# Kernel tuning notes

Hardware: AMD Instinct MI355X
Metric: run time of the kernel (lower is better)

## Reference

```python
import itertools
import jax, jax.numpy as jnp
import numpy as np

N_FEATURES = 32
DEGREE = 3
BATCH = 32768


def poly_feature_indices(n_features: int, degree: int):
    indices = []
    for d in range(1, degree + 1):
        for combo in itertools.combinations_with_replacement(range(n_features), d):
            indices.append(combo)
    return indices


def padded_index_matrix(n_features: int, degree: int) -> np.ndarray:
    # Pad each monomial index tuple to length `degree` with the sentinel
    # index n_features, which points at a column of ones appended to x.
    idx_list = poly_feature_indices(n_features, degree)
    mat = np.full((len(idx_list), degree), n_features, dtype=np.int32)
    for i, tup in enumerate(idx_list):
        mat[i, : len(tup)] = tup
    return mat


def setup_inputs() -> dict:
    key = jax.random.key(0)
    k1, k2, k3 = jax.random.split(key, 3)
    n_poly = len(poly_feature_indices(N_FEATURES, DEGREE))  # 6544
    x = jax.random.normal(k1, (BATCH, N_FEATURES), dtype=jnp.float32)
    # nn.Linear(n_poly, 1) init scale
    bound = 1.0 / np.sqrt(n_poly)
    W = jax.random.uniform(k2, (1, n_poly), dtype=jnp.float32, minval=-bound, maxval=bound)
    b = jax.random.uniform(k3, (1,), dtype=jnp.float32, minval=-bound, maxval=bound)
    idx = jnp.asarray(padded_index_matrix(N_FEATURES, DEGREE))  # (n_poly, degree) int32
    return {"x": x, "W": W, "b": b, "idx": idx}


def reference(x, W, b, idx):
    # Append a ones column so the sentinel index acts as multiplicative identity.
    x_aug = jnp.concatenate([x, jnp.ones((x.shape[0], 1), dtype=x.dtype)], axis=1)
    # z[b, p] = prod_k x_aug[b, idx[p, k]]  -> (batch, n_poly)
    z = x_aug[:, idx[:, 0]]
    for k in range(1, idx.shape[1]):  # small fixed loop over degree
        z = z * x_aug[:, idx[:, k]]
    # Linear(n_poly, 1): z @ W.T + b
    return z @ W.T + b
```

## Files before the change

kernel.cpp:

```cpp
#include <hip/hip_runtime.h>


__device__ __forceinline__ constexpr int off2(int a, int b) {
    return 32 + 32 * a - (a * (a - 1)) / 2 + (b - a);
}

__device__ __forceinline__ constexpr int off3(int a, int b, int c) {
    constexpr int g3[32] = {
        0,    528,  1024, 1489, 1924, 2330, 2708, 3059,
        3384, 3684, 3960, 4213, 4444, 4654, 4844, 5015,
        5168, 5304, 5424, 5529, 5620, 5698, 5764, 5819,
        5864, 5900, 5928, 5949, 5964, 5974, 5980, 5983};
    return 560 + g3[a] + 32 * (b - a) - ((b * (b - 1)) / 2 - (a * (a - 1)) / 2) + (c - b);
}

template <int A0, int A1>
__device__ __forceinline__ float eval_range(const float* __restrict__ W,
                                            const float (&x)[32]) {
    float acc = 0.0f;
#pragma unroll
    for (int a = A0; a < A1; ++a) {
        const float xa = x[a];
        acc = __builtin_fmaf(W[a], xa, acc);
#pragma unroll
        for (int b = a; b < 32; ++b) {
            const float pab = xa * x[b];
            float S = W[off2(a, b)];
#pragma unroll
            for (int c = b; c < 32; ++c) {
                S = __builtin_fmaf(W[off3(a, b, c)], x[c], S);
            }
            acc = __builtin_fmaf(pab, S, acc);
        }
    }
    return acc;
}

__global__ __launch_bounds__(256) void PolyLinear_40218073760341_kernel(
    const float* __restrict__ X,
    const float* __restrict__ W,
    const float* __restrict__ Bp,
    float* __restrict__ out)
{
    const int lane = threadIdx.x & 63;
    const int wave = threadIdx.x >> 6;
    const int row  = blockIdx.x * 64 + lane;

    float x[32];
    const float4* xr = (const float4*)(X + (long)row * 32);
#pragma unroll
    for (int i = 0; i < 8; ++i) {
        const float4 v = xr[i];
        x[4 * i + 0] = v.x;
        x[4 * i + 1] = v.y;
        x[4 * i + 2] = v.z;
        x[4 * i + 3] = v.w;
    }

    float acc;
    if (wave == 0)      acc = eval_range<0, 3>(W, x);
    else if (wave == 1) acc = eval_range<3, 7>(W, x);
    else if (wave == 2) acc = eval_range<7, 12>(W, x);
    else                acc = eval_range<12, 32>(W, x);

    __shared__ float partial[4][64];
    partial[wave][lane] = acc;
    __syncthreads();

    if (wave == 0) {
        const float r = partial[0][lane] + partial[1][lane] +
                        partial[2][lane] + partial[3][lane] + Bp[0];
        out[row] = r;
    }
}

extern "C" void kernel_launch(void* const* d_in, const int* in_sizes, int n_in,
                              void* d_out, int out_size, void* d_ws, size_t ws_size,
                              hipStream_t stream) {
    const float* X  = (const float*)d_in[0];
    const float* W  = (const float*)d_in[1];
    const float* Bp = (const float*)d_in[2];
    float* out = (float*)d_out;

    const int rows = in_sizes[0] / 32;
    const int grid = rows / 64;
    PolyLinear_40218073760341_kernel<<<grid, 256, 0, stream>>>(X, W, Bp, out);
}
```

Measured before the change: 82.31 us.

## Stage weights in LDS and have each wave evaluate two rows over 16 balanced parts

Weights are staged into shared memory once per block instead of being read through scalar/global loads. Each block now uses 16 waves that split the (a,b) monomial pairs into 16 roughly equal chunks by cumulative cubic count. Each lane evaluates two rows at once, so every loaded weight is used twice. The cost is a 26KB LDS footprint per block, LDS reads in place of broadcast scalar loads, and higher register pressure from holding two 32-float rows.

```diff
diff --git a/kernel.cpp b/kernel.cpp
--- a/kernel.cpp
+++ b/kernel.cpp
@@ -1,5 +1,8 @@
 #include <hip/hip_runtime.h>
 
+
+#define NPART 16
+#define TOTAL3 5984
 
 __device__ __forceinline__ constexpr int off2(int a, int b) {
     return 32 + 32 * a - (a * (a - 1)) / 2 + (b - a);
@@ -14,29 +17,52 @@
     return 560 + g3[a] + 32 * (b - a) - ((b * (b - 1)) / 2 - (a * (a - 1)) / 2) + (c - b);
 }
 
-template <int A0, int A1>
-__device__ __forceinline__ float eval_range(const float* __restrict__ W,
-                                            const float (&x)[32]) {
-    float acc = 0.0f;
+__device__ __forceinline__ constexpr int cum3(int a, int b) {
+    return off3(a, b, b) - 560;
+}
+
+__device__ __forceinline__ constexpr int owner_of(int a, int b) {
+    return (cum3(a, b) * NPART) / TOTAL3;
+}
+
+template <int PART>
+__device__ __forceinline__ void eval_part(const float* __restrict__ Wl,
+                                          const float (&x0)[32],
+                                          const float (&x1)[32],
+                                          float& acc0, float& acc1) {
+    float a0 = 0.0f, a1 = 0.0f;
 #pragma unroll
-    for (int a = A0; a < A1; ++a) {
-        const float xa = x[a];
-        acc = __builtin_fmaf(W[a], xa, acc);
+    for (int a = 0; a < 32; ++a) {
 #pragma unroll
         for (int b = a; b < 32; ++b) {
-            const float pab = xa * x[b];
-            float S = W[off2(a, b)];
+            const int own = owner_of(a, b);
+            if (own == PART) {
+                const float xa0 = x0[a], xa1 = x1[a];
+                if (a == b) {
+                    const float w1 = Wl[a];
+                    a0 = __builtin_fmaf(w1, xa0, a0);
+                    a1 = __builtin_fmaf(w1, xa1, a1);
+                }
+                float s0 = Wl[off2(a, b)];
+                float s1 = s0;
 #pragma unroll
-            for (int c = b; c < 32; ++c) {
-                S = __builtin_fmaf(W[off3(a, b, c)], x[c], S);
+                for (int c = b; c < 32; ++c) {
+                    const float w = Wl[off3(a, b, c)];
+                    s0 = __builtin_fmaf(w, x0[c], s0);
+                    s1 = __builtin_fmaf(w, x1[c], s1);
+                }
+                const float p0 = xa0 * x0[b];
+                const float p1 = xa1 * x1[b];
+                a0 = __builtin_fmaf(p0, s0, a0);
+                a1 = __builtin_fmaf(p1, s1, a1);
             }
-            acc = __builtin_fmaf(pab, S, acc);
         }
     }
-    return acc;
+    acc0 = a0;
+    acc1 = a1;
 }
 
-__global__ __launch_bounds__(256) void PolyLinear_40218073760341_kernel(
+__global__ __launch_bounds__(1024, 4) void PolyLinear_40218073760341_kernel(
     const float* __restrict__ X,
     const float* __restrict__ W,
     const float* __restrict__ Bp,
@@ -44,33 +70,52 @@
 {
     const int lane = threadIdx.x & 63;
     const int wave = threadIdx.x >> 6;
-    const int row  = blockIdx.x * 64 + lane;
+    const long base = (long)blockIdx.x * 128;
 
-    float x[32];
-    const float4* xr = (const float4*)(X + (long)row * 32);
-#pragma unroll
-    for (int i = 0; i < 8; ++i) {
-        const float4 v = xr[i];
-        x[4 * i + 0] = v.x;
-        x[4 * i + 1] = v.y;
-        x[4 * i + 2] = v.z;
-        x[4 * i + 3] = v.w;
+    __shared__ float Wl[6544];
+    __shared__ float partial[16][128];
+
+    {
+        const float4* Wg = (const float4*)W;
+        float4* Wd = (float4*)Wl;
+        for (int i = threadIdx.x; i < 1636; i += 1024) Wd[i] = Wg[i];
     }
 
-    float acc;
-    if (wave == 0)      acc = eval_range<0, 3>(W, x);
-    else if (wave == 1) acc = eval_range<3, 7>(W, x);
-    else if (wave == 2) acc = eval_range<7, 12>(W, x);
-    else                acc = eval_range<12, 32>(W, x);
-
-    __shared__ float partial[4][64];
-    partial[wave][lane] = acc;
+    float x0[32], x1[32];
+    {
+        const float4* xr0 = (const float4*)(X + (base + lane) * 32);
+        const float4* xr1 = (const float4*)(X + (base + 64 + lane) * 32);
+#pragma unroll
+        for (int i = 0; i < 8; ++i) {
+            const float4 v = xr0[i];
+            x0[4 * i + 0] = v.x; x0[4 * i + 1] = v.y;
+            x0[4 * i + 2] = v.z; x0[4 * i + 3] = v.w;
+            const float4 u = xr1[i];
+            x1[4 * i + 0] = u.x; x1[4 * i + 1] = u.y;
+            x1[4 * i + 2] = u.z; x1[4 * i + 3] = u.w;
+        }
+    }
     __syncthreads();
 
-    if (wave == 0) {
-        const float r = partial[0][lane] + partial[1][lane] +
-                        partial[2][lane] + partial[3][lane] + Bp[0];
-        out[row] = r;
+    float acc0 = 0.0f, acc1 = 0.0f;
+#define EVAL_CASE(P) case P: eval_part<P>(Wl, x0, x1, acc0, acc1); break;
+    switch (wave) {
+        EVAL_CASE(0)  EVAL_CASE(1)  EVAL_CASE(2)  EVAL_CASE(3)
+        EVAL_CASE(4)  EVAL_CASE(5)  EVAL_CASE(6)  EVAL_CASE(7)
+        EVAL_CASE(8)  EVAL_CASE(9)  EVAL_CASE(10) EVAL_CASE(11)
+        EVAL_CASE(12) EVAL_CASE(13) EVAL_CASE(14) EVAL_CASE(15)
+    }
+#undef EVAL_CASE
+
+    partial[wave][lane] = acc0;
+    partial[wave][64 + lane] = acc1;
+    __syncthreads();
+
+    if (threadIdx.x < 128) {
+        float r = Bp[0];
+#pragma unroll
+        for (int w = 0; w < 16; ++w) r += partial[w][threadIdx.x];
+        out[base + threadIdx.x] = r;
     }
 }
 
@@ -83,6 +128,6 @@
     float* out = (float*)d_out;
 
     const int rows = in_sizes[0] / 32;
-    const int grid = rows / 64;
-    PolyLinear_40218073760341_kernel<<<grid, 256, 0, stream>>>(X, W, Bp, out);
+    const int grid = rows / 128;
+    PolyLinear_40218073760341_kernel<<<grid, 1024, 0, stream>>>(X, W, Bp, out);
 }
```

Result: slower. 112.3 us (+36.4%).
